# Performance work log

Measured on AMD Instinct MI355X. Metric: run time of the kernel, lower is better.

The kernel has to match this reference:

```python
import jax, jax.numpy as jnp
import numpy as np

N_NODES = 256
COND = 64
ARCH = [256, 512, 1024]
E = N_NODES * (N_NODES - 1) // 2  # 32640 upper-triangular edges
OUT = 2 * E                        # 65280 final-layer width
B = 512
CUTOFF = 0.0
TAU = 1.0


def _make_params(key, dims):
    ws, bs = [], []
    for i, (din, dout) in enumerate(zip(dims[:-1], dims[1:])):
        k = jax.random.fold_in(key, i)
        kw, kb = jax.random.split(k)
        ws.append(jax.random.normal(kw, (din, dout), jnp.float32) * 0.02)
        bs.append(jax.random.normal(kb, (dout,), jnp.float32) * 0.02)
    return ws, bs


def setup_inputs() -> dict:
    key = jax.random.key(0)
    kx, kg, kbig, ksmall = jax.random.split(key, 4)
    x = jax.random.normal(kx, (B, COND), jnp.float32)
    gumbel = jax.random.gumbel(kg, (B, E, 2), jnp.float32)
    dims = [COND] + ARCH + [OUT]
    bw, bb = _make_params(kbig, dims)
    sw, sb = _make_params(ksmall, dims)
    inp = {"x": x, "gumbel": gumbel}
    for i in range(4):
        inp[f"bw{i}"] = bw[i]; inp[f"bb{i}"] = bb[i]
        inp[f"sw{i}"] = sw[i]; inp[f"sb{i}"] = sb[i]
    return inp


def _expert_adj(x, ws, bs, gumbel):
    # MLP: relu on all but last layer
    h = x
    for w, b in zip(ws[:-1], bs[:-1]):
        h = jax.nn.relu(h @ w + b)
    logits = (h @ ws[-1] + bs[-1]).reshape(x.shape[0], E, 2)
    # hard gumbel-softmax (straight-through), tau=1
    g = (logits + gumbel) / TAU
    y_soft = jax.nn.softmax(g, axis=-1)
    y_hard = jax.nn.one_hot(jnp.argmax(g, axis=-1), 2, dtype=y_soft.dtype)
    y = y_hard + y_soft - jax.lax.stop_gradient(y_soft)
    x0 = y[:, :, 0]  # [B, E]
    iu, ju = jnp.triu_indices(N_NODES, k=1)
    adj = jnp.zeros((x.shape[0], N_NODES, N_NODES), x0.dtype)
    adj = adj.at[:, iu, ju].set(x0)
    return adj + jnp.swapaxes(adj, 1, 2)


def reference(x, gumbel,
              bw0, bb0, bw1, bb1, bw2, bb2, bw3, bb3,
              sw0, sb0, sw1, sb1, sw2, sb2, sw3, sb3):
    big_ws, big_bs = [bw0, bw1, bw2, bw3], [bb0, bb1, bb2, bb3]
    small_ws, small_bs = [sw0, sw1, sw2, sw3], [sb0, sb1, sb2, sb3]
    adj_big = _expert_adj(x, big_ws, big_bs, gumbel)
    adj_small = _expert_adj(x, small_ws, small_bs, gumbel)
    mask_big = x[:, 0] > CUTOFF  # [B]
    out = jnp.where(mask_big[:, None, None], adj_big, adj_small)
    return out
```

## Files before the change

### kernel.cpp

```cpp
#include <hip/hip_runtime.h>

#define N_NODES 256
#define COND    64
#define E_PAIRS 32640
#define OUTCOLS 65280
#define BATCH   512
#define SLOTS   576
#define D1      256
#define D2      512
#define D3      1024

typedef __attribute__((ext_vector_type(8))) short bf16x8;
typedef __attribute__((ext_vector_type(4))) float f32x4;
typedef __attribute__((ext_vector_type(4))) unsigned int u32x4;

static __device__ __forceinline__ unsigned short f2bf(float f) {
    unsigned int u = __float_as_uint(f);
    u += 0x7FFF + ((u >> 16) & 1);
    return (unsigned short)(u >> 16);
}
static __device__ __forceinline__ float bf2f(unsigned short h) {
    return __uint_as_float(((unsigned int)h) << 16);
}

static __device__ __forceinline__ void gload_lds16(const float* g, float* l) {
    __builtin_amdgcn_global_load_lds(
        (const __attribute__((address_space(1))) unsigned int*)g,
        (__attribute__((address_space(3))) unsigned int*)l,
        16, 0, 0);
}

__global__ void k0_sort(const float* __restrict__ x, int* __restrict__ meta,
                        int* __restrict__ borig) {
    __shared__ int wc[9];
    int t = threadIdx.x;
    if (t < SLOTS) borig[t] = -1;
    int m = 0;
    if (t < BATCH) m = (x[t * COND] > 0.0f) ? 1 : 0;
    unsigned long long bm = __ballot(m);
    int wave = t >> 6;
    int lane = t & 63;
    int lanePre = __popcll(bm & ((1ull << lane) - 1ull));
    if (lane == 0) wc[wave] = __popcll(bm);
    __syncthreads();
    int nbig = 0, preBig = 0;
    #pragma unroll
    for (int w = 0; w < 8; ++w) {
        int c = wc[w];
        if (w < wave) preBig += c;
        nbig += c;
    }
    int S = (nbig + 63) & ~63;
    if (t < BATCH) {
        int onesBefore = preBig + lanePre;
        int slot = m ? onesBefore : (S + (t - onesBefore));
        borig[slot] = t;
    }
    if (t == 0) meta[0] = S;
}

template <bool GATHER, int K, int DOUT, bool SPLIT>
__global__ __launch_bounds__(256) void k1_gemm(
    const float* __restrict__ in,
    const float* __restrict__ wbig, const float* __restrict__ bbig,
    const float* __restrict__ wsml, const float* __restrict__ bsml,
    const int* __restrict__ meta, const int* __restrict__ borig,
    float* __restrict__ out, unsigned short* __restrict__ hbA) {
    __shared__ float hs[16][64 + 4];
    __shared__ float wt[16][64 + 4];
    int tid = threadIdx.x;
    int by = blockIdx.x;
    int bx = blockIdx.y;
    int r0 = by * 64;
    int cb = bx * 64;
    int S = meta[0];
    bool big = (r0 < S);
    const float* w = big ? wbig : wsml;
    const float* bias = big ? bbig : bsml;

    int lm = tid >> 2;
    int lq = tid & 3;
    int wk = tid >> 4;
    int wc = (tid & 15) * 4;

    int tm = tid >> 4;
    int tn = tid & 15;

    const float* hrow;
    if (GATHER) {
        int b = borig[r0 + lm];
        hrow = (b >= 0) ? &in[(size_t)b * K] : (const float*)0;
    } else {
        hrow = &in[(size_t)(r0 + lm) * K];
    }

    float acc[4][4];
    #pragma unroll
    for (int i = 0; i < 4; ++i)
        #pragma unroll
        for (int j = 0; j < 4; ++j) acc[i][j] = 0.f;

    for (int k0 = 0; k0 < K; k0 += 16) {
        float4 hv = make_float4(0.f, 0.f, 0.f, 0.f);
        if (!GATHER || hrow) hv = *(const float4*)&hrow[k0 + lq * 4];
        float4 wv = *(const float4*)&w[(size_t)(k0 + wk) * DOUT + cb + wc];
        __syncthreads();
        hs[lq * 4 + 0][lm] = hv.x;
        hs[lq * 4 + 1][lm] = hv.y;
        hs[lq * 4 + 2][lm] = hv.z;
        hs[lq * 4 + 3][lm] = hv.w;
        *(float4*)&wt[wk][wc] = wv;
        __syncthreads();
        #pragma unroll
        for (int kk = 0; kk < 16; ++kk) {
            float4 a  = *(const float4*)&hs[kk][tm * 4];
            float4 bf = *(const float4*)&wt[kk][tn * 4];
            acc[0][0] = fmaf(a.x, bf.x, acc[0][0]);
            acc[0][1] = fmaf(a.x, bf.y, acc[0][1]);
            acc[0][2] = fmaf(a.x, bf.z, acc[0][2]);
            acc[0][3] = fmaf(a.x, bf.w, acc[0][3]);
            acc[1][0] = fmaf(a.y, bf.x, acc[1][0]);
            acc[1][1] = fmaf(a.y, bf.y, acc[1][1]);
            acc[1][2] = fmaf(a.y, bf.z, acc[1][2]);
            acc[1][3] = fmaf(a.y, bf.w, acc[1][3]);
            acc[2][0] = fmaf(a.z, bf.x, acc[2][0]);
            acc[2][1] = fmaf(a.z, bf.y, acc[2][1]);
            acc[2][2] = fmaf(a.z, bf.z, acc[2][2]);
            acc[2][3] = fmaf(a.z, bf.w, acc[2][3]);
            acc[3][0] = fmaf(a.w, bf.x, acc[3][0]);
            acc[3][1] = fmaf(a.w, bf.y, acc[3][1]);
            acc[3][2] = fmaf(a.w, bf.z, acc[3][2]);
            acc[3][3] = fmaf(a.w, bf.w, acc[3][3]);
        }
    }

    float4 bv = *(const float4*)&bias[cb + tn * 4];
    #pragma unroll
    for (int i = 0; i < 4; ++i) {
        float o[4];
        o[0] = fmaxf(acc[i][0] + bv.x, 0.f);
        o[1] = fmaxf(acc[i][1] + bv.y, 0.f);
        o[2] = fmaxf(acc[i][2] + bv.z, 0.f);
        o[3] = fmaxf(acc[i][3] + bv.w, 0.f);
        if (SPLIT) {
            int row = r0 + tm * 4 + i;
            int by_ = row >> 6, rl = row & 63;
            int mfr = rl >> 4, p15 = rl & 15;
            int kt  = cb + tn * 4;
            int kk  = kt >> 5, lgk = (kt >> 3) & 3, j0 = kt & 7;
            size_t base = (size_t)(by_ * 32 + kk) * 6144 + (size_t)mfr * 512
                        + (size_t)(lgk * 16 + p15) * 8 + j0;
            ushort4 s0, s1, s2;
            unsigned short* q0[4] = {&s0.x, &s0.y, &s0.z, &s0.w};
            unsigned short* q1[4] = {&s1.x, &s1.y, &s1.z, &s1.w};
            unsigned short* q2[4] = {&s2.x, &s2.y, &s2.z, &s2.w};
            #pragma unroll
            for (int j = 0; j < 4; ++j) {
                unsigned short a0 = f2bf(o[j]);
                float r1v = o[j] - bf2f(a0);
                unsigned short a1 = f2bf(r1v);
                float r2v = r1v - bf2f(a1);
                *q0[j] = a0; *q1[j] = a1; *q2[j] = f2bf(r2v);
            }
            *(ushort4*)&hbA[base]        = s0;
            *(ushort4*)&hbA[base + 2048] = s1;
            *(ushort4*)&hbA[base + 4096] = s2;
        } else {
            float4 ov;
            ov.x = o[0]; ov.y = o[1]; ov.z = o[2]; ov.w = o[3];
            *(float4*)&out[(size_t)(r0 + tm * 4 + i) * DOUT + cb + tn * 4] = ov;
        }
    }
}

__global__ __launch_bounds__(256) void k2_mfma(
    const unsigned short* __restrict__ hbA,
    const float* __restrict__ bw3, const float* __restrict__ bb3,
    const float* __restrict__ sw3, const float* __restrict__ sb3,
    const float* __restrict__ gum,
    const int* __restrict__ meta, const int* __restrict__ borig,
    unsigned char* __restrict__ bits) {
    __shared__ float Braw[2][32][256];

    int tid = threadIdx.x;
    int wgid = blockIdx.x;
    int xr  = wgid & 7;
    int s_  = wgid >> 3;
    int by  = s_ % 9;
    int q   = s_ / 9;
    int bx  = q * 8 + xr;
    if (bx >= 255) return;

    int r0 = by * 64;
    int cb = bx * 256;
    int db = bx * 128;
    int S = meta[0];
    bool big = (r0 < S);
    const float* w3 = big ? bw3 : sw3;
    const float* b3 = big ? bb3 : sb3;

    int lane = tid & 63;
    int wid  = tid >> 6;
    int l15  = lane & 15;
    int lg   = lane >> 4;

    f32x4 acc[4][2];
    #pragma unroll
    for (int m = 0; m < 4; ++m)
        #pragma unroll
        for (int n = 0; n < 2; ++n) acc[m][n] = (f32x4)0.f;

    const unsigned short* ap0 = hbA + (size_t)(by * 32) * 6144 + (size_t)lane * 8;
    const float* wtile = w3 + cb;

#define STAGE(BUF, T) do {                                                      \
    _Pragma("unroll")                                                           \
    for (int rr_ = 0; rr_ < 8; ++rr_) {                                         \
        int row_ = wid * 8 + rr_;                                               \
        gload_lds16(wtile + (size_t)((T) * 32 + row_) * OUTCOLS + lane * 4,     \
                    &Braw[BUF][row_][0]);                                       \
    }                                                                           \
} while (0)

#define STEP(BUF, T) do {                                                       \
    const unsigned short* ap_ = ap0 + (size_t)(T) * 6144;                       \
    bf16x8 af_[3][4];                                                           \
    _Pragma("unroll")                                                           \
    for (int l_ = 0; l_ < 3; ++l_)                                              \
        _Pragma("unroll")                                                       \
        for (int m_ = 0; m_ < 4; ++m_)                                          \
            af_[l_][m_] = *(const bf16x8*)(ap_ + l_ * 2048 + m_ * 512);         \
    _Pragma("unroll")                                                           \
    for (int n_ = 0; n_ < 2; ++n_) {                                            \
        int fi_ = wid * 64 + n_ * 32 + l15 * 2;  \
        u32x4 f0_, f1_, f2_;                                                    \
        _Pragma("unroll")                                                       \
        for (int w_ = 0; w_ < 4; ++w_) {                                        \
            float2 pA_ = *(const float2*)&Braw[BUF][lg * 8 + 2 * w_][fi_];      \
            float2 pB_ = *(const float2*)&Braw[BUF][lg * 8 + 2 * w_ + 1][fi_];  \
            float dA_ = pA_.x - pA_.y;                                          \
            float dB_ = pB_.x - pB_.y;                                          \
            unsigned short aL_ = f2bf(dA_), aH_ = f2bf(dB_);                    \
            f0_[w_] = (unsigned int)aL_ | ((unsigned int)aH_ << 16);            \
            float rA_ = dA_ - bf2f(aL_), rB_ = dB_ - bf2f(aH_);                 \
            unsigned short bL_ = f2bf(rA_), bH_ = f2bf(rB_);                    \
            f1_[w_] = (unsigned int)bL_ | ((unsigned int)bH_ << 16);            \
            float sA_ = rA_ - bf2f(bL_), sB_ = rB_ - bf2f(bH_);                 \
            f2_[w_] = (unsigned int)f2bf(sA_) | ((unsigned int)f2bf(sB_) << 16);\
        }                                                                       \
        bf16x8 b0_ = __builtin_bit_cast(bf16x8, f0_);                           \
        bf16x8 b1_ = __builtin_bit_cast(bf16x8, f1_);                           \
        bf16x8 b2_ = __builtin_bit_cast(bf16x8, f2_);                           \
        _Pragma("unroll")                                                       \
        for (int m_ = 0; m_ < 4; ++m_) {                                        \
            f32x4 c_ = acc[m_][n_];                                             \
            c_ = __builtin_amdgcn_mfma_f32_16x16x32_bf16(af_[0][m_], b0_, c_, 0, 0, 0); \
            c_ = __builtin_amdgcn_mfma_f32_16x16x32_bf16(af_[0][m_], b1_, c_, 0, 0, 0); \
            c_ = __builtin_amdgcn_mfma_f32_16x16x32_bf16(af_[1][m_], b0_, c_, 0, 0, 0); \
            c_ = __builtin_amdgcn_mfma_f32_16x16x32_bf16(af_[1][m_], b1_, c_, 0, 0, 0); \
            c_ = __builtin_amdgcn_mfma_f32_16x16x32_bf16(af_[0][m_], b2_, c_, 0, 0, 0); \
            c_ = __builtin_amdgcn_mfma_f32_16x16x32_bf16(af_[2][m_], b0_, c_, 0, 0, 0); \
            acc[m_][n_] = c_;                                                   \
        }                                                                       \
    }                                                                           \
} while (0)

    STAGE(0, 0);
    __syncthreads();
    for (int t = 0; t < 32; ++t) {
        int buf = t & 1;
        if (t < 31) STAGE(buf ^ 1, t + 1);
        STEP(buf, t);
        __syncthreads();
    }
#undef STAGE
#undef STEP

    #pragma unroll
    for (int n = 0; n < 2; ++n) {
        int colg = db + wid * 32 + n * 16 + l15;
        float2 bv = *(const float2*)&b3[2 * colg];
        float bd = bv.x - bv.y;
        #pragma unroll
        for (int m = 0; m < 4; ++m) {
            #pragma unroll
            for (int r = 0; r < 4; ++r) {
                int slot = r0 + m * 16 + lg * 4 + r;
                int b = borig[slot];
                if (b < 0) continue;
                float2 gv = *(const float2*)&gum[(size_t)b * OUTCOLS + 2 * colg];
                float g = acc[m][n][r] + bd + (gv.x - gv.y);
                bits[(size_t)b * E_PAIRS + colg] = (g >= 0.f) ? 1 : 0;
            }
        }
    }
}

__global__ __launch_bounds__(256) void k3_expand(
    const unsigned char* __restrict__ bits, float* __restrict__ out) {
    __shared__ unsigned char L[64][68];
    const int ti_tab[10] = {0,0,0,0,1,1,1,2,2,3};
    const int tj_tab[10] = {0,1,2,3,1,2,3,2,3,3};
    int p = blockIdx.x;
    int b = blockIdx.y;
    int ti = ti_tab[p], tj = tj_tab[p];
    int t = threadIdx.x;

    {
        int r = t >> 2;
        int q = t & 3;
        int i = ti * 64 + r;
        long base = (long)b * E_PAIRS + (long)i * (511 - i) / 2 - i - 1;
        int j0 = tj * 64 + q * 16;
        #pragma unroll
        for (int k = 0; k < 16; ++k) {
            int j = j0 + k;
            unsigned char v = (j > i) ? bits[base + j] : (unsigned char)0;
            L[r][q * 16 + k] = v;
        }
    }
    __syncthreads();

    int h  = t >> 4;
    int w4 = (t & 15) * 4;

    {
        #pragma unroll
        for (int rr = 0; rr < 4; ++rr) {
            int ii = rr * 16 + h;
            int i_ = ti * 64 + ii;
            float4 v;
            if (ti == tj) {
                int jj;
                jj = w4 + 0; v.x = (jj > ii) ? (float)L[ii][jj] : (jj < ii ? (float)L[jj][ii] : 0.f);
                jj = w4 + 1; v.y = (jj > ii) ? (float)L[ii][jj] : (jj < ii ? (float)L[jj][ii] : 0.f);
                jj = w4 + 2; v.z = (jj > ii) ? (float)L[ii][jj] : (jj < ii ? (float)L[jj][ii] : 0.f);
                jj = w4 + 3; v.w = (jj > ii) ? (float)L[ii][jj] : (jj < ii ? (float)L[jj][ii] : 0.f);
            } else {
                v.x = (float)L[ii][w4 + 0];
                v.y = (float)L[ii][w4 + 1];
                v.z = (float)L[ii][w4 + 2];
                v.w = (float)L[ii][w4 + 3];
            }
            size_t o = (((size_t)b * 256 + i_) * 256) + tj * 64 + w4;
            *(float4*)&out[o] = v;
        }
    }

    if (ti != tj) {
        #pragma unroll
        for (int rr = 0; rr < 4; ++rr) {
            int jj = rr * 16 + h;
            int j_ = tj * 64 + jj;
            float4 v;
            v.x = (float)L[w4 + 0][jj];
            v.y = (float)L[w4 + 1][jj];
            v.z = (float)L[w4 + 2][jj];
            v.w = (float)L[w4 + 3][jj];
            size_t o = (((size_t)b * 256 + j_) * 256) + ti * 64 + w4;
            *(float4*)&out[o] = v;
        }
    }
}

extern "C" void kernel_launch(void* const* d_in, const int* in_sizes, int n_in,
                              void* d_out, int out_size, void* d_ws, size_t ws_size,
                              hipStream_t stream) {
    const float* x   = (const float*)d_in[0];
    const float* gum = (const float*)d_in[1];
    const float* bw0 = (const float*)d_in[2];  const float* bb0 = (const float*)d_in[3];
    const float* sw0 = (const float*)d_in[4];  const float* sb0 = (const float*)d_in[5];
    const float* bw1 = (const float*)d_in[6];  const float* bb1 = (const float*)d_in[7];
    const float* sw1 = (const float*)d_in[8];  const float* sb1 = (const float*)d_in[9];
    const float* bw2 = (const float*)d_in[10]; const float* bb2 = (const float*)d_in[11];
    const float* sw2 = (const float*)d_in[12]; const float* sb2 = (const float*)d_in[13];
    const float* bw3 = (const float*)d_in[14]; const float* bb3 = (const float*)d_in[15];
    const float* sw3 = (const float*)d_in[16]; const float* sb3 = (const float*)d_in[17];

    char* ws = (char*)d_ws;
    int*   meta  = (int*)ws;
    int*   borig = (int*)(ws + 64);
    float* act1  = (float*)(ws + 4096);
    float* act2  = (float*)(ws + 593920);
    unsigned short* hbA = (unsigned short*)(ws + 1773568);
    unsigned char* bits = (unsigned char*)(ws + 5312512);
    float* out = (float*)d_out;

    k0_sort<<<1, SLOTS, 0, stream>>>(x, meta, borig);
    k1_gemm<true,  COND, D1, false><<<dim3(9, D1 / 64), 256, 0, stream>>>(
        x,    bw0, bb0, sw0, sb0, meta, borig, act1, 0);
    k1_gemm<false, D1,   D2, false><<<dim3(9, D2 / 64), 256, 0, stream>>>(
        act1, bw1, bb1, sw1, sb1, meta, borig, act2, 0);
    k1_gemm<false, D2,   D3, true><<<dim3(9, D3 / 64), 256, 0, stream>>>(
        act2, bw2, bb2, sw2, sb2, meta, borig, (float*)0, hbA);
    k2_mfma<<<2304, 256, 0, stream>>>(hbA, bw3, bb3, sw3, sb3, gum,
                                      meta, borig, bits);
    k3_expand<<<dim3(10, BATCH), 256, 0, stream>>>(bits, out);
}
```

Baseline: 1.070 ms.

## Halve k2 column tile, stage A into LDS, triple-buffer-style async pipeline

The final-layer MFMA kernel now uses 128-column tiles instead of 256 and launches twice as many workgroups. The A operand (bf16 hidden activations) is also staged into LDS with async global-to-LDS loads, rather than read directly from global memory. Loads run two tiles ahead with explicit vmcnt waits and raw s_barriers instead of __syncthreads, so memory latency overlaps compute. k3's lookup tables are replaced with arithmetic. The smaller tile doubles the reads of A and lowers per-block reuse, but it should improve occupancy and load balance.

New measurement: 1.105 ms. +3.3%, slower.

```diff
diff --git a/kernel.cpp b/kernel.cpp
--- a/kernel.cpp
+++ b/kernel.cpp
@@ -9,6 +9,7 @@
 #define D1      256
 #define D2      512
 #define D3      1024
+#define NT      32
 
 typedef __attribute__((ext_vector_type(8))) short bf16x8;
 typedef __attribute__((ext_vector_type(4))) float f32x4;
@@ -180,20 +181,20 @@
     const float* __restrict__ gum,
     const int* __restrict__ meta, const int* __restrict__ borig,
     unsigned char* __restrict__ bits) {
-    __shared__ float Braw[2][32][256];
+    __shared__ float Bs[2][32][128];
+    __shared__ unsigned short As[2][6144];
 
     int tid = threadIdx.x;
     int wgid = blockIdx.x;
-    int xr  = wgid & 7;
-    int s_  = wgid >> 3;
-    int by  = s_ % 9;
-    int q   = s_ / 9;
-    int bx  = q * 8 + xr;
-    if (bx >= 255) return;
+    int xr = wgid & 7;
+    int z  = wgid >> 3;
+    int by = z % 9;
+    int q  = z / 9;
+    int ct = q * 8 + xr;
+    if (ct >= 510) return;
 
     int r0 = by * 64;
-    int cb = bx * 256;
-    int db = bx * 128;
+    int cb = ct * 128;
     int S = meta[0];
     bool big = (r0 < S);
     const float* w3 = big ? bw3 : sw3;
@@ -204,94 +205,97 @@
     int l15  = lane & 15;
     int lg   = lane >> 4;
 
-    f32x4 acc[4][2];
+    f32x4 acc[4];
     #pragma unroll
-    for (int m = 0; m < 4; ++m)
-        #pragma unroll
-        for (int n = 0; n < 2; ++n) acc[m][n] = (f32x4)0.f;
-
-    const unsigned short* ap0 = hbA + (size_t)(by * 32) * 6144 + (size_t)lane * 8;
-    const float* wtile = w3 + cb;
+    for (int m = 0; m < 4; ++m) acc[m] = (f32x4)0.f;
+
+    const unsigned short* hA = hbA + (size_t)(by * 32) * 6144;
 
 #define STAGE(BUF, T) do {                                                      \
     _Pragma("unroll")                                                           \
-    for (int rr_ = 0; rr_ < 8; ++rr_) {                                         \
-        int row_ = wid * 8 + rr_;                                               \
-        gload_lds16(wtile + (size_t)((T) * 32 + row_) * OUTCOLS + lane * 4,     \
-                    &Braw[BUF][row_][0]);                                       \
+    for (int d_ = 0; d_ < 4; ++d_) {                                            \
+        int row_ = wid * 8 + 2 * d_;                                            \
+        gload_lds16(w3 + (size_t)((T) * 32 + row_ + (lane >> 5)) * OUTCOLS      \
+                        + cb + (lane & 31) * 4,                                 \
+                    &Bs[BUF][row_][0]);                                         \
+    }                                                                           \
+    _Pragma("unroll")                                                           \
+    for (int c_ = 0; c_ < 3; ++c_) {                                            \
+        int ch_ = wid * 3 + c_;                                                 \
+        gload_lds16((const float*)(hA + (size_t)(T) * 6144 + ch_ * 512          \
+                                   + lane * 8),                                 \
+                    (float*)&As[BUF][ch_ * 512]);                               \
     }                                                                           \
 } while (0)
 
-#define STEP(BUF, T) do {                                                       \
-    const unsigned short* ap_ = ap0 + (size_t)(T) * 6144;                       \
+#define COMPUTE(BUF) do {                                                       \
     bf16x8 af_[3][4];                                                           \
     _Pragma("unroll")                                                           \
     for (int l_ = 0; l_ < 3; ++l_)                                              \
         _Pragma("unroll")                                                       \
         for (int m_ = 0; m_ < 4; ++m_)                                          \
-            af_[l_][m_] = *(const bf16x8*)(ap_ + l_ * 2048 + m_ * 512);         \
+            af_[l_][m_] = *(const bf16x8*)&As[BUF][l_ * 2048 + m_ * 512 + lane * 8]; \
+    u32x4 f0_, f1_, f2_;                                                        \
     _Pragma("unroll")                                                           \
-    for (int n_ = 0; n_ < 2; ++n_) {                                            \
-        int fi_ = wid * 64 + n_ * 32 + l15 * 2;  \
-        u32x4 f0_, f1_, f2_;                                                    \
-        _Pragma("unroll")                                                       \
-        for (int w_ = 0; w_ < 4; ++w_) {                                        \
-            float2 pA_ = *(const float2*)&Braw[BUF][lg * 8 + 2 * w_][fi_];      \
-            float2 pB_ = *(const float2*)&Braw[BUF][lg * 8 + 2 * w_ + 1][fi_];  \
-            float dA_ = pA_.x - pA_.y;                                          \
-            float dB_ = pB_.x - pB_.y;                                          \
-            unsigned short aL_ = f2bf(dA_), aH_ = f2bf(dB_);                    \
-            f0_[w_] = (unsigned int)aL_ | ((unsigned int)aH_ << 16);            \
-            float rA_ = dA_ - bf2f(aL_), rB_ = dB_ - bf2f(aH_);                 \
-            unsigned short bL_ = f2bf(rA_), bH_ = f2bf(rB_);                    \
-            f1_[w_] = (unsigned int)bL_ | ((unsigned int)bH_ << 16);            \
-            float sA_ = rA_ - bf2f(bL_), sB_ = rB_ - bf2f(bH_);                 \
-            f2_[w_] = (unsigned int)f2bf(sA_) | ((unsigned int)f2bf(sB_) << 16);\
-        }                                                                       \
-        bf16x8 b0_ = __builtin_bit_cast(bf16x8, f0_);                           \
-        bf16x8 b1_ = __builtin_bit_cast(bf16x8, f1_);                           \
-        bf16x8 b2_ = __builtin_bit_cast(bf16x8, f2_);                           \
-        _Pragma("unroll")                                                       \
-        for (int m_ = 0; m_ < 4; ++m_) {                                        \
-            f32x4 c_ = acc[m_][n_];                                             \
-            c_ = __builtin_amdgcn_mfma_f32_16x16x32_bf16(af_[0][m_], b0_, c_, 0, 0, 0); \
-            c_ = __builtin_amdgcn_mfma_f32_16x16x32_bf16(af_[0][m_], b1_, c_, 0, 0, 0); \
-            c_ = __builtin_amdgcn_mfma_f32_16x16x32_bf16(af_[1][m_], b0_, c_, 0, 0, 0); \
-            c_ = __builtin_amdgcn_mfma_f32_16x16x32_bf16(af_[1][m_], b1_, c_, 0, 0, 0); \
-            c_ = __builtin_amdgcn_mfma_f32_16x16x32_bf16(af_[0][m_], b2_, c_, 0, 0, 0); \
-            c_ = __builtin_amdgcn_mfma_f32_16x16x32_bf16(af_[2][m_], b0_, c_, 0, 0, 0); \
-            acc[m_][n_] = c_;                                                   \
-        }                                                                       \
+    for (int p_ = 0; p_ < 4; ++p_) {                                            \
+        float2 pa_ = *(const float2*)&Bs[BUF][lg * 8 + 2 * p_][wid * 32 + l15 * 2];     \
+        float2 pb_ = *(const float2*)&Bs[BUF][lg * 8 + 2 * p_ + 1][wid * 32 + l15 * 2]; \
+        float dA_ = pa_.x - pa_.y, dB_ = pb_.x - pb_.y;                         \
+        unsigned short aL_ = f2bf(dA_), aH_ = f2bf(dB_);                        \
+        f0_[p_] = (unsigned)aL_ | ((unsigned)aH_ << 16);                        \
+        float rA_ = dA_ - bf2f(aL_), rB_ = dB_ - bf2f(aH_);                     \
+        unsigned short bL_ = f2bf(rA_), bH_ = f2bf(rB_);                        \
+        f1_[p_] = (unsigned)bL_ | ((unsigned)bH_ << 16);                        \
+        float sA_ = rA_ - bf2f(bL_), sB_ = rB_ - bf2f(bH_);                     \
+        f2_[p_] = (unsigned)f2bf(sA_) | ((unsigned)f2bf(sB_) << 16);            \
+    }                                                                           \
+    bf16x8 b0_ = __builtin_bit_cast(bf16x8, f0_);                               \
+    bf16x8 b1_ = __builtin_bit_cast(bf16x8, f1_);                               \
+    bf16x8 b2_ = __builtin_bit_cast(bf16x8, f2_);                               \
+    _Pragma("unroll")                                                           \
+    for (int m_ = 0; m_ < 4; ++m_) {                                            \
+        f32x4 c_ = acc[m_];                                                     \
+        c_ = __builtin_amdgcn_mfma_f32_16x16x32_bf16(af_[0][m_], b0_, c_, 0, 0, 0); \
+        c_ = __builtin_amdgcn_mfma_f32_16x16x32_bf16(af_[0][m_], b1_, c_, 0, 0, 0); \
+        c_ = __builtin_amdgcn_mfma_f32_16x16x32_bf16(af_[1][m_], b0_, c_, 0, 0, 0); \
+        c_ = __builtin_amdgcn_mfma_f32_16x16x32_bf16(af_[1][m_], b1_, c_, 0, 0, 0); \
+        c_ = __builtin_amdgcn_mfma_f32_16x16x32_bf16(af_[0][m_], b2_, c_, 0, 0, 0); \
+        c_ = __builtin_amdgcn_mfma_f32_16x16x32_bf16(af_[2][m_], b0_, c_, 0, 0, 0); \
+        acc[m_] = c_;                                                           \
     }                                                                           \
 } while (0)
 
     STAGE(0, 0);
-    __syncthreads();
-    for (int t = 0; t < 32; ++t) {
-        int buf = t & 1;
-        if (t < 31) STAGE(buf ^ 1, t + 1);
-        STEP(buf, t);
-        __syncthreads();
+    STAGE(1, 1);
+    for (int t = 0; t < NT; ++t) {
+        if (t < NT - 1) {
+            asm volatile("s_waitcnt vmcnt(7)" ::: "memory");
+        } else {
+            asm volatile("s_waitcnt vmcnt(0)" ::: "memory");
+        }
+        __builtin_amdgcn_s_barrier();
+        __builtin_amdgcn_sched_barrier(0);
+        COMPUTE(t & 1);
+        __builtin_amdgcn_s_barrier();
+        __builtin_amdgcn_sched_barrier(0);
+        if (t + 2 < NT) STAGE(t & 1, t + 2);
     }
 #undef STAGE
-#undef STEP
-
+#undef COMPUTE
+
+    int colg = ct * 64 + wid * 16 + l15;
+    float2 bv = *(const float2*)&b3[2 * colg];
+    float bd = bv.x - bv.y;
     #pragma unroll
-    for (int n = 0; n < 2; ++n) {
-        int colg = db + wid * 32 + n * 16 + l15;
-        float2 bv = *(const float2*)&b3[2 * colg];
-        float bd = bv.x - bv.y;
-        #pragma unroll
-        for (int m = 0; m < 4; ++m) {
-            #pragma unroll
-            for (int r = 0; r < 4; ++r) {
-                int slot = r0 + m * 16 + lg * 4 + r;
-                int b = borig[slot];
-                if (b < 0) continue;
-                float2 gv = *(const float2*)&gum[(size_t)b * OUTCOLS + 2 * colg];
-                float g = acc[m][n][r] + bd + (gv.x - gv.y);
-                bits[(size_t)b * E_PAIRS + colg] = (g >= 0.f) ? 1 : 0;
-            }
+    for (int m = 0; m < 4; ++m) {
+        #pragma unroll
+        for (int r = 0; r < 4; ++r) {
+            int slot = r0 + m * 16 + lg * 4 + r;
+            int b = borig[slot];
+            if (b < 0) continue;
+            float2 gv = *(const float2*)&gum[(size_t)b * OUTCOLS + 2 * colg];
+            float g = acc[m][r] + bd + (gv.x - gv.y);
+            bits[(size_t)b * E_PAIRS + colg] = (g >= 0.f) ? 1 : 0;
         }
     }
 }
@@ -299,11 +303,11 @@
 __global__ __launch_bounds__(256) void k3_expand(
     const unsigned char* __restrict__ bits, float* __restrict__ out) {
     __shared__ unsigned char L[64][68];
-    const int ti_tab[10] = {0,0,0,0,1,1,1,2,2,3};
-    const int tj_tab[10] = {0,1,2,3,1,2,3,2,3,3};
     int p = blockIdx.x;
+    int ti = (p >= 4) + (p >= 7) + (p >= 9);
+    int off = (ti == 0) ? 0 : (ti == 1) ? 4 : (ti == 2) ? 7 : 9;
+    int tj = ti + (p - off);
     int b = blockIdx.y;
-    int ti = ti_tab[p], tj = tj_tab[p];
     int t = threadIdx.x;
 
     {
@@ -393,7 +397,7 @@
         act1, bw1, bb1, sw1, sb1, meta, borig, act2, 0);
     k1_gemm<false, D2,   D3, true><<<dim3(9, D3 / 64), 256, 0, stream>>>(
         act2, bw2, bb2, sw2, sb2, meta, borig, (float*)0, hbA);
-    k2_mfma<<<2304, 256, 0, stream>>>(hbA, bw3, bb3, sw3, sb3, gum,
+    k2_mfma<<<4608, 256, 0, stream>>>(hbA, bw3, bb3, sw3, sb3, gum,
                                       meta, borig, bits);
     k3_expand<<<dim3(10, BATCH), 256, 0, stream>>>(bits, out);
 }
```
